# Optimization experiments

Measured on AMD Instinct MI355X. Metric: run time of the kernel, lower is better.

## Reference

```python
import jax, jax.numpy as jnp
import numpy as np
import math

B, S, H = 1, 2048, 4096
NH, HD = 32, 128  # heads, head_dim
ROPE_THETA = 10000.0
SINK = 4
RECENT_RATIO = 0.1


def setup_inputs() -> dict:
    key = jax.random.key(0)
    ks = jax.random.split(key, 5)
    scale = 0.02
    return {
        "hidden_states": jax.random.normal(ks[0], (B, S, H), jnp.float32),
        "Wq": jax.random.normal(ks[1], (H, H), jnp.float32) * scale,
        "Wk": jax.random.normal(ks[2], (H, H), jnp.float32) * scale,
        "Wv": jax.random.normal(ks[3], (H, H), jnp.float32) * scale,
        "Wo": jax.random.normal(ks[4], (H, H), jnp.float32) * scale,
        "position_ids": jnp.arange(S, dtype=jnp.int64)[None, :],
    }


def _rope(x, cos, sin):
    # x: [B, NH, S, HD]; rotate_half = cat(-x2, x1)
    half = x.shape[-1] // 2
    rot = jnp.concatenate([-x[..., half:], x[..., :half]], axis=-1)
    return x * cos + rot * sin


def reference(hidden_states, Wq, Wk, Wv, Wo, position_ids):
    b, s, h = hidden_states.shape
    # projections (torch Linear: x @ W^T), split heads -> [B, NH, S, HD]
    q = (hidden_states @ Wq.T).reshape(b, s, NH, HD).transpose(0, 2, 1, 3)
    k = (hidden_states @ Wk.T).reshape(b, s, NH, HD).transpose(0, 2, 1, 3)
    v = (hidden_states @ Wv.T).reshape(b, s, NH, HD).transpose(0, 2, 1, 3)

    # rotary embeddings from position_ids
    inv_freq = 1.0 / (ROPE_THETA ** (jnp.arange(0, HD, 2, dtype=jnp.float32) / HD))
    freqs = position_ids.astype(jnp.float32)[..., None] * inv_freq  # [B, S, HD/2]
    emb = jnp.concatenate([freqs, freqs], axis=-1)                   # [B, S, HD]
    cos = jnp.cos(emb)[:, None, :, :]
    sin = jnp.sin(emb)[:, None, :, :]
    q = _rope(q, cos, sin)
    k = _rope(k, cos, sin)

    # causal attention
    scores = jnp.einsum('bhqd,bhkd->bhqk', q, k) / math.sqrt(HD)
    neg = jnp.finfo(scores.dtype).min
    causal = jnp.tril(jnp.ones((s, s), dtype=bool))
    scores = jnp.where(causal[None, None], scores, neg)
    attn = jax.nn.softmax(scores, axis=-1)
    out = jnp.einsum('bhqk,bhkd->bhqd', attn, v)
    out = out.transpose(0, 2, 1, 3).reshape(b, s, h)
    attn_output = out @ Wo.T

    # H2O streaming cache eviction: sink (first 4) + recent window KV
    recent = int(s * RECENT_RATIO)
    k_evicted = jnp.concatenate([k[:, :, :SINK, :], k[:, :, s - recent:, :]], axis=2)
    v_evicted = jnp.concatenate([v[:, :, :SINK, :], v[:, :, s - recent:, :]], axis=2)
    return attn_output, k_evicted, v_evicted
```

## Files before the change

kernel.cpp:

```cpp
#include <hip/hip_runtime.h>
#include <hip/hip_bf16.h>

typedef __bf16 bf16;
typedef __bf16 bf16x4 __attribute__((ext_vector_type(4)));
typedef __bf16 bf16x8 __attribute__((ext_vector_type(8)));
typedef float f32x4 __attribute__((ext_vector_type(4)));

#define MFMA16(a, b, c) __builtin_amdgcn_mfma_f32_16x16x32_bf16(a, b, c, 0, 0, 0)

constexpr int S_LEN = 2048;
constexpr int HDIM = 4096;
constexpr int NHEADS = 32;
constexpr int HEADD = 128;
constexpr int SINKN = 4;
constexpr int RECENT = 204;
constexpr int EVROWS = SINKN + RECENT;
constexpr float QSCALE = 0.08838834764831845f;

constexpr int JOBS_PER_HEAD = 40;
constexpr int SLOTS_PER_HEAD = 36;
constexpr size_t SLOT_BYTES = 33792;

__device__ inline bf16x8 cvt8(const float* p) {
    float4 a = *(const float4*)p;
    float4 b = *(const float4*)(p + 4);
    return bf16x8{(bf16)a.x, (bf16)a.y, (bf16)a.z, (bf16)a.w,
                  (bf16)b.x, (bf16)b.y, (bf16)b.z, (bf16)b.w};
}

__device__ inline void gload16(const bf16* g, bf16* l) {
    __builtin_amdgcn_global_load_lds(
        (const __attribute__((address_space(1))) unsigned int*)g,
        (__attribute__((address_space(3))) unsigned int*)l, 16, 0, 0);
}

__global__ __launch_bounds__(256) void cvt_kernel(const float* __restrict__ in,
                                                  bf16* __restrict__ out, int n8) {
    int i = blockIdx.x * 256 + threadIdx.x;
    if (i >= n8) return;
    *(bf16x8*)(out + (size_t)i * 8) = cvt8(in + (size_t)i * 8);
}

__device__ __forceinline__ void stage_b256(const bf16* __restrict__ Bp, bf16* dst,
                                           int K, int kc, int tid) {
#pragma unroll
    for (int r = 0; r < 2; ++r) {
        int idx = r * 512 + tid;
        int row = idx >> 3;
        int gs = (idx & 7) ^ (row & 7);
        gload16(Bp + (size_t)row * K + kc + gs * 8, dst + idx * 8);
    }
}
template <int MH>
__device__ __forceinline__ void stage_a256(const bf16* __restrict__ Ap, bf16* dst,
                                           int K, int kc, int tid) {
#pragma unroll
    for (int r = 0; r < 2; ++r) {
        int idx = r * 512 + tid;
        int row = idx >> 3;
        int gs = (idx & 7) ^ (row & 7);
        gload16(Ap + (size_t)(MH * 128 + row) * K + kc + gs * 8,
                dst + MH * 8192 + idx * 8);
    }
}
template <int MH>
__device__ __forceinline__ void lda256(const bf16* buf, int wm, int lg, int lr,
                                       bf16x8 (&af)[2][2]) {
#pragma unroll
    for (int mt = 0; mt < 2; ++mt)
#pragma unroll
        for (int kk = 0; kk < 2; ++kk)
            af[mt][kk] = *(const bf16x8*)&buf[MH * 8192 + (wm * 32 + mt * 16 + lr) * 64 +
                                              (((kk * 4 + lg) ^ (lr & 7)) * 8)];
}
__device__ __forceinline__ void ldb256(const bf16* buf, int wn, int lg, int lr,
                                       bf16x8 (&bfr)[4][2]) {
#pragma unroll
    for (int nt = 0; nt < 4; ++nt)
#pragma unroll
        for (int kk = 0; kk < 2; ++kk)
            bfr[nt][kk] = *(const bf16x8*)&buf[(wn * 64 + nt * 16 + lr) * 64 +
                                               (((kk * 4 + lg) ^ (lr & 7)) * 8)];
}
template <int MH>
__device__ __forceinline__ void mma256(const bf16x8 (&af)[2][2], const bf16x8 (&bfr)[4][2],
                                       f32x4 (&acc)[2][2][4]) {
#pragma unroll
    for (int mt = 0; mt < 2; ++mt)
#pragma unroll
        for (int nt = 0; nt < 4; ++nt)
#pragma unroll
            for (int kk = 0; kk < 2; ++kk)
                acc[MH][mt][nt] = MFMA16(af[mt][kk], bfr[nt][kk], acc[MH][mt][nt]);
}

template <bool C_IS_F32>
__global__ __launch_bounds__(512, 2) void gemm256(const bf16* __restrict__ A,
                                                  const bf16* __restrict__ B,
                                                  void* __restrict__ Cv,
                                                  int M, int N, int K) {
    __shared__ bf16 Abuf[2][256 * 64];
    __shared__ bf16 Bbuf[2][128 * 64];

    const int tid = threadIdx.x;
    const int lane = tid & 63, wid = tid >> 6;
    const int wm = wid >> 1, wn = wid & 1;
    const int lg = lane >> 4, lr = lane & 15;

    const int bid = blockIdx.x;
    const int bx = (bid & 7) * 4 + (bid >> 6);
    const int by = (bid >> 3) & 7;
    const int m0 = by * 256, n0 = bx * 128;

    const bf16* Ap = A + (size_t)m0 * K;
    const bf16* Bp = B + (size_t)n0 * K;

    f32x4 acc[2][2][4] = {};
    bf16x8 af[2][2], bfr[4][2];

    stage_b256(Bp, Bbuf[0], K, 0, tid);
    stage_a256<0>(Ap, Abuf[0], K, 0, tid);
    stage_a256<1>(Ap, Abuf[0], K, 0, tid);
    asm volatile("s_waitcnt vmcnt(2)" ::: "memory");
    __builtin_amdgcn_s_barrier();

    const bf16 *Ard = Abuf[0], *Brd = Bbuf[0];
    bf16 *Awr = Abuf[1], *Bwr = Bbuf[1];

    const int NT = K / 64;
    for (int t = 0; t < NT - 1; ++t) {
        const int kc = (t + 1) * 64;
        ldb256(Brd, wn, lg, lr, bfr);
        lda256<0>(Ard, wm, lg, lr, af);
        stage_b256(Bp, Bwr, K, kc, tid);
        stage_a256<0>(Ap, Awr, K, kc, tid);
        __builtin_amdgcn_s_barrier();
        asm volatile("s_waitcnt lgkmcnt(0)" ::: "memory");
        __builtin_amdgcn_sched_barrier(0);
        __builtin_amdgcn_s_setprio(1);
        mma256<0>(af, bfr, acc);
        __builtin_amdgcn_s_setprio(0);
        asm volatile("s_waitcnt vmcnt(4)" ::: "memory");
        __builtin_amdgcn_s_barrier();
        lda256<1>(Ard, wm, lg, lr, af);
        stage_a256<1>(Ap, Awr, K, kc, tid);
        __builtin_amdgcn_s_barrier();
        asm volatile("s_waitcnt lgkmcnt(0)" ::: "memory");
        __builtin_amdgcn_sched_barrier(0);
        __builtin_amdgcn_s_setprio(1);
        mma256<1>(af, bfr, acc);
        __builtin_amdgcn_s_setprio(0);
        asm volatile("s_waitcnt vmcnt(2)" ::: "memory");
        __builtin_amdgcn_s_barrier();
        const bf16* tA = Ard; Ard = Awr; Awr = (bf16*)tA;
        const bf16* tB = Brd; Brd = Bwr; Bwr = (bf16*)tB;
    }
    asm volatile("s_waitcnt vmcnt(0)" ::: "memory");
    __builtin_amdgcn_s_barrier();
    ldb256(Brd, wn, lg, lr, bfr);
    lda256<0>(Ard, wm, lg, lr, af);
    mma256<0>(af, bfr, acc);
    lda256<1>(Ard, wm, lg, lr, af);
    mma256<1>(af, bfr, acc);

#pragma unroll
    for (int mh = 0; mh < 2; ++mh)
#pragma unroll
        for (int mt = 0; mt < 2; ++mt)
#pragma unroll
            for (int nt = 0; nt < 4; ++nt)
#pragma unroll
                for (int r = 0; r < 4; ++r) {
                    int row = m0 + mh * 128 + wm * 32 + mt * 16 + lg * 4 + r;
                    int col = n0 + wn * 64 + nt * 16 + lr;
                    if constexpr (C_IS_F32)
                        ((float*)Cv)[(size_t)row * N + col] = acc[mh][mt][nt][r];
                    else
                        ((bf16*)Cv)[(size_t)row * N + col] = (bf16)acc[mh][mt][nt][r];
                }
}

__global__ __launch_bounds__(256) void rope_kernel(bf16* __restrict__ q,
                                                   bf16* __restrict__ k) {
    const int s = blockIdx.x;
    const int t = threadIdx.x;
    const int hh = t >> 3;
    const int i0 = (t & 7) << 3;
    const size_t base = (size_t)s * HDIM + hh * HEADD;

    bf16x8 q1 = *(bf16x8*)(q + base + i0);
    bf16x8 q2 = *(bf16x8*)(q + base + 64 + i0);
    bf16x8 k1 = *(bf16x8*)(k + base + i0);
    bf16x8 k2 = *(bf16x8*)(k + base + 64 + i0);
    bf16x8 q1o, q2o, k1o, k2o;
    const float pos = (float)s;
#pragma unroll
    for (int j = 0; j < 8; ++j) {
        float f = pos * exp2f((float)(i0 + j) * (-0.2076205059304602f));
        float sn, cs;
        sincosf(f, &sn, &cs);
        float x1 = (float)q1[j], x2 = (float)q2[j];
        q1o[j] = (bf16)((x1 * cs - x2 * sn) * QSCALE);
        q2o[j] = (bf16)((x2 * cs + x1 * sn) * QSCALE);
        x1 = (float)k1[j]; x2 = (float)k2[j];
        k1o[j] = (bf16)(x1 * cs - x2 * sn);
        k2o[j] = (bf16)(x2 * cs + x1 * sn);
    }
    *(bf16x8*)(q + base + i0) = q1o;
    *(bf16x8*)(q + base + 64 + i0) = q2o;
    *(bf16x8*)(k + base + i0) = k1o;
    *(bf16x8*)(k + base + 64 + i0) = k2o;
}

__global__ __launch_bounds__(256) void transpose_v(const bf16* __restrict__ v,
                                                   bf16* __restrict__ vt) {
    __shared__ bf16 tile[64][136];
    const int h = blockIdx.x;
    const int s0 = blockIdx.y * 64;
    const int tid = threadIdx.x;
#pragma unroll
    for (int j = 0; j < 4; ++j) {
        int ch = tid + 256 * j;
        int row = ch >> 4, c8 = (ch & 15) << 3;
        *(bf16x8*)&tile[row][c8] =
            *(const bf16x8*)(v + (size_t)(s0 + row) * HDIM + h * HEADD + c8);
    }
    __syncthreads();
#pragma unroll
    for (int j = 0; j < 4; ++j) {
        int ch = tid + 256 * j;
        int d = ch >> 3, s8 = (ch & 7) << 3;
        bf16x8 w;
#pragma unroll
        for (int i = 0; i < 8; ++i) w[i] = tile[s8 + i][d];
        *(bf16x8*)(vt + ((size_t)h * HEADD + d) * S_LEN + s0 + s8) = w;
    }
}

__global__ __launch_bounds__(256, 2) void attn_kernel(const bf16* __restrict__ q,
                                                      const bf16* __restrict__ k,
                                                      const bf16* __restrict__ vt,
                                                      bf16* __restrict__ o,
                                                      char* __restrict__ partials) {
    __shared__ bf16 K_lds[2][64 * 128];
    __shared__ bf16 V_lds[128 * 64];
    __shared__ bf16 P_lds[4][32 * 72];

    const int tid = threadIdx.x;
    const int lane = tid & 63, wid = tid >> 6;
    const int lg = lane >> 4, lr = lane & 15;

    const int bj = blockIdx.x;
    const int h = bj / JOBS_PER_HEAD;
    const int within = JOBS_PER_HEAD - 1 - (bj % JOBS_PER_HEAD);
    int qb, chunk, nj;
    if (within < 4)       { qb = within; chunk = 0; nj = 1; }
    else if (within < 12) { int u2 = within - 4;  qb = 4  + (u2 >> 1); chunk = u2 & 1;        nj = 2; }
    else if (within < 24) { int u2 = within - 12; int q3 = u2 / 3; qb = 8 + q3; chunk = u2 - 3 * q3; nj = 3; }
    else                  { int u2 = within - 24; qb = 12 + (u2 >> 2); chunk = u2 & 3;        nj = 4; }
    const int q0 = qb * 128;
    const int ntiles = 2 * qb + 2;
    const int tb = chunk * 8;
    const int te = min(tb + 8, ntiles);

    bf16x8 aq[2][4];
#pragma unroll
    for (int rs = 0; rs < 2; ++rs)
#pragma unroll
        for (int dc = 0; dc < 4; ++dc)
            aq[rs][dc] = *(const bf16x8*)(q + (size_t)(q0 + wid * 32 + rs * 16 + lr) * HDIM +
                                          h * HEADD + dc * 32 + lg * 8);

    f32x4 oacc[2][8] = {};
    float m_[2] = {-1e30f, -1e30f};
    float l_[2] = {0.f, 0.f};
    bf16* pw = &P_lds[wid][0];

    {
        const int kv0 = tb << 6;
#pragma unroll
        for (int i = 0; i < 4; ++i) {
            const int c = wid * 4 + i;
            const int krow = 4 * c + (lane >> 4);
            const int kg = (lane & 15) ^ (krow & 7);
            gload16(k + (size_t)(kv0 + krow) * HDIM + h * HEADD + kg * 8,
                    &K_lds[0][c * 512]);
        }
    }

    int cur = 0;
    for (int t = tb; t < te; ++t) {
        const int kv0 = t << 6;
#pragma unroll
        for (int i = 0; i < 4; ++i) {
            const int c = wid * 4 + i;
            const int vrow = 8 * c + (lane >> 3);
            const int vg = (lane & 7) ^ (vrow & 7);
            gload16(vt + (size_t)(h * HEADD + vrow) * S_LEN + kv0 + vg * 8,
                    &V_lds[c * 512]);
        }
        if (t + 1 < te) {
            const int kvn = (t + 1) << 6;
#pragma unroll
            for (int i = 0; i < 4; ++i) {
                const int c = wid * 4 + i;
                const int krow = 4 * c + (lane >> 4);
                const int kg = (lane & 15) ^ (krow & 7);
                gload16(k + (size_t)(kvn + krow) * HDIM + h * HEADD + kg * 8,
                        &K_lds[cur ^ 1][c * 512]);
            }
            asm volatile("s_waitcnt vmcnt(8)" ::: "memory");
        } else {
            asm volatile("s_waitcnt vmcnt(4)" ::: "memory");
        }
        __builtin_amdgcn_s_barrier();
        __builtin_amdgcn_sched_barrier(0);

        const bf16* Kb = &K_lds[cur][0];
        f32x4 st[2][4] = {};
#pragma unroll
        for (int kt = 0; kt < 4; ++kt) {
            bf16x8 kf[4];
#pragma unroll
            for (int dc = 0; dc < 4; ++dc)
                kf[dc] = *(const bf16x8*)&Kb[(kt * 16 + lr) * 128 +
                                             (((dc * 4 + lg) ^ (lr & 7)) * 8)];
#pragma unroll
            for (int dc = 0; dc < 4; ++dc) {
                st[0][kt] = MFMA16(kf[dc], aq[0][dc], st[0][kt]);
                st[1][kt] = MFMA16(kf[dc], aq[1][dc], st[1][kt]);
            }
        }

#pragma unroll
        for (int rs = 0; rs < 2; ++rs) {
            const int qr0 = q0 + wid * 32 + rs * 16;
            float v[16];
            if ((kv0 + 63) > qr0) {
                const int qidx = qr0 + lr;
#pragma unroll
                for (int kt = 0; kt < 4; ++kt)
#pragma unroll
                    for (int r = 0; r < 4; ++r) {
                        float x = st[rs][kt][r];
                        if (kv0 + kt * 16 + lg * 4 + r > qidx) x = -1e30f;
                        v[kt * 4 + r] = x;
                    }
            } else {
#pragma unroll
                for (int kt = 0; kt < 4; ++kt)
#pragma unroll
                    for (int r = 0; r < 4; ++r) v[kt * 4 + r] = st[rs][kt][r];
            }
            float pm = v[0];
#pragma unroll
            for (int i = 1; i < 16; ++i) pm = fmaxf(pm, v[i]);
            pm = fmaxf(pm, __shfl_xor(pm, 16));
            pm = fmaxf(pm, __shfl_xor(pm, 32));

            if (__any(pm > m_[rs] + 8.0f)) {
                float mn = fmaxf(m_[rs], pm);
                float sc = __expf(m_[rs] - mn);
                m_[rs] = mn;
                l_[rs] *= sc;
                float scb[4];
#pragma unroll
                for (int r = 0; r < 4; ++r)
                    scb[r] = __uint_as_float(__builtin_amdgcn_ds_bpermute(
                        (lg * 4 + r) * 4, __float_as_uint(sc)));
#pragma unroll
                for (int dt = 0; dt < 8; ++dt)
#pragma unroll
                    for (int r = 0; r < 4; ++r) oacc[rs][dt][r] *= scb[r];
            }
            const float mn = m_[rs];
            float rsum = 0.f;
#pragma unroll
            for (int kt = 0; kt < 4; ++kt) {
                bf16x4 pk;
#pragma unroll
                for (int r = 0; r < 4; ++r) {
                    float p = __expf(v[kt * 4 + r] - mn);
                    rsum += p;
                    pk[r] = (bf16)p;
                }
                *(bf16x4*)&pw[(rs * 16 + lr) * 72 + kt * 16 + lg * 4] = pk;
            }
            rsum += __shfl_xor(rsum, 16);
            rsum += __shfl_xor(rsum, 32);
            l_[rs] += rsum;
        }

        if (t + 1 < te) asm volatile("s_waitcnt vmcnt(4)" ::: "memory");
        else            asm volatile("s_waitcnt vmcnt(0)" ::: "memory");
        __builtin_amdgcn_s_barrier();
        __builtin_amdgcn_sched_barrier(0);

        bf16x8 pa[2][2];
#pragma unroll
        for (int rs = 0; rs < 2; ++rs)
#pragma unroll
            for (int kt2 = 0; kt2 < 2; ++kt2)
                pa[rs][kt2] = *(const bf16x8*)&pw[(rs * 16 + lr) * 72 + kt2 * 32 + lg * 8];
#pragma unroll
        for (int kt2 = 0; kt2 < 2; ++kt2)
#pragma unroll
            for (int dt = 0; dt < 8; ++dt) {
                bf16x8 bv = *(const bf16x8*)&V_lds[(dt * 16 + lr) * 64 +
                                                   (((kt2 * 4 + lg) ^ (lr & 7)) * 8)];
                oacc[0][dt] = MFMA16(pa[0][kt2], bv, oacc[0][dt]);
                oacc[1][dt] = MFMA16(pa[1][kt2], bv, oacc[1][dt]);
            }

        __builtin_amdgcn_s_barrier();
        __builtin_amdgcn_sched_barrier(0);
        cur ^= 1;
    }

    if (nj == 1) {
#pragma unroll
        for (int rs = 0; rs < 2; ++rs) {
            float lb[4];
#pragma unroll
            for (int r = 0; r < 4; ++r)
                lb[r] = __uint_as_float(__builtin_amdgcn_ds_bpermute(
                    (lg * 4 + r) * 4, __float_as_uint(l_[rs])));
#pragma unroll
            for (int r = 0; r < 4; ++r) {
                float inv = 1.0f / lb[r];
                const int row = q0 + wid * 32 + rs * 16 + lg * 4 + r;
#pragma unroll
                for (int dt = 0; dt < 8; ++dt)
                    o[(size_t)row * HDIM + h * HEADD + dt * 16 + lr] =
                        (bf16)(oacc[rs][dt][r] * inv);
            }
        }
    } else {
        const int sb = (qb < 8) ? (qb - 4) * 2 : (qb < 12) ? 8 + (qb - 8) * 3
                                                           : 20 + (qb - 12) * 4;
        char* slotp = partials + ((size_t)h * SLOTS_PER_HEAD + sb + chunk) * SLOT_BYTES;
        bf16* Op = (bf16*)slotp;
        float* mp = (float*)(slotp + 32768);
        float* lp = mp + 128;
#pragma unroll
        for (int rs = 0; rs < 2; ++rs) {
            const int rowl = wid * 32 + rs * 16;
#pragma unroll
            for (int r = 0; r < 4; ++r)
#pragma unroll
                for (int dt = 0; dt < 8; ++dt)
                    Op[(rowl + lg * 4 + r) * HEADD + dt * 16 + lr] = (bf16)oacc[rs][dt][r];
            if (lg == 0) { mp[rowl + lr] = m_[rs]; lp[rowl + lr] = l_[rs]; }
        }
    }
}

__global__ __launch_bounds__(256) void combine_kernel(const char* __restrict__ partials,
                                                      bf16* __restrict__ o) {
    const int h = blockIdx.x;
    const int qb = 4 + blockIdx.y;
    const int nj = (2 * qb + 9) / 8;
    const int sb = (qb < 8) ? (qb - 4) * 2 : (qb < 12) ? 8 + (qb - 8) * 3
                                                       : 20 + (qb - 12) * 4;
    const char* base = partials + ((size_t)h * SLOTS_PER_HEAD + sb) * SLOT_BYTES;

    const int row = threadIdx.x >> 1;
    const int d0 = (threadIdx.x & 1) * 64;

    float mc[4], lc[4];
    float M = -1e30f;
    for (int c = 0; c < nj; ++c) {
        const char* sp = base + (size_t)c * SLOT_BYTES;
        mc[c] = ((const float*)(sp + 32768))[row];
        lc[c] = ((const float*)(sp + 33280))[row];
        M = fmaxf(M, mc[c]);
    }
    float denom = 0.f;
    float acc[64] = {};
    for (int c = 0; c < nj; ++c) {
        float wgt = __expf(mc[c] - M);
        denom += wgt * lc[c];
        const bf16* Op = (const bf16*)(base + (size_t)c * SLOT_BYTES);
#pragma unroll
        for (int j = 0; j < 8; ++j) {
            bf16x8 a = *(const bf16x8*)&Op[row * HEADD + d0 + j * 8];
#pragma unroll
            for (int e = 0; e < 8; ++e) acc[j * 8 + e] += wgt * (float)a[e];
        }
    }
    float inv = 1.0f / denom;
    bf16* dst = o + (size_t)(qb * 128 + row) * HDIM + h * HEADD + d0;
#pragma unroll
    for (int j = 0; j < 8; ++j) {
        bf16x8 w;
#pragma unroll
        for (int e = 0; e < 8; ++e) w[e] = (bf16)(acc[j * 8 + e] * inv);
        *(bf16x8*)&dst[j * 8] = w;
    }
}

__global__ __launch_bounds__(256) void evict_kernel(const bf16* __restrict__ k,
                                                    const bf16* __restrict__ v,
                                                    float* __restrict__ out) {
    const int total = NHEADS * EVROWS * HEADD;
    int idx = blockIdx.x * 256 + threadIdx.x;
    if (idx >= 2 * total) return;
    const int which = idx / total;
    const int rem = idx % total;
    const int hh = rem / (EVROWS * HEADD);
    const int i = (rem / HEADD) % EVROWS;
    const int d = rem % HEADD;
    const int s = (i < SINKN) ? i : (S_LEN - RECENT) + (i - SINKN);
    const bf16* src = which ? v : k;
    out[(size_t)S_LEN * HDIM + (size_t)which * total + rem] =
        (float)src[(size_t)s * HDIM + hh * HEADD + d];
}

extern "C" void kernel_launch(void* const* d_in, const int* in_sizes, int n_in,
                              void* d_out, int out_size, void* d_ws, size_t ws_size,
                              hipStream_t stream) {
    const float* hs = (const float*)d_in[0];
    const float* Wq = (const float*)d_in[1];
    const float* Wk = (const float*)d_in[2];
    const float* Wv = (const float*)d_in[3];
    const float* Wo = (const float*)d_in[4];
    float* out = (float*)d_out;

    const size_t MB = 1024 * 1024;
    char* w = (char*)d_ws;
    bf16* hs_bf = (bf16*)(w);
    bf16* W_bf  = (bf16*)(w + 16 * MB);
    char* part  = w;
    bf16* q_ws  = (bf16*)(w + 48 * MB);
    bf16* k_ws  = (bf16*)(w + 64 * MB);
    bf16* v_ws  = (bf16*)(w + 80 * MB);
    bf16* vt_ws = (bf16*)(w + 96 * MB);
    bf16* o_ws  = q_ws;

    const int nW8 = HDIM * HDIM / 8;
    const int nH8 = S_LEN * HDIM / 8;

    cvt_kernel<<<(nH8 + 255) / 256, 256, 0, stream>>>(hs, hs_bf, nH8);

    cvt_kernel<<<(nW8 + 255) / 256, 256, 0, stream>>>(Wq, W_bf, nW8);
    gemm256<false><<<256, 512, 0, stream>>>(hs_bf, W_bf, q_ws, S_LEN, HDIM, HDIM);
    cvt_kernel<<<(nW8 + 255) / 256, 256, 0, stream>>>(Wk, W_bf, nW8);
    gemm256<false><<<256, 512, 0, stream>>>(hs_bf, W_bf, k_ws, S_LEN, HDIM, HDIM);
    cvt_kernel<<<(nW8 + 255) / 256, 256, 0, stream>>>(Wv, W_bf, nW8);
    gemm256<false><<<256, 512, 0, stream>>>(hs_bf, W_bf, v_ws, S_LEN, HDIM, HDIM);

    rope_kernel<<<S_LEN, 256, 0, stream>>>(q_ws, k_ws);
    transpose_v<<<dim3(NHEADS, S_LEN / 64), 256, 0, stream>>>(v_ws, vt_ws);

    evict_kernel<<<(2 * NHEADS * EVROWS * HEADD + 255) / 256, 256, 0, stream>>>(k_ws, v_ws, out);

    attn_kernel<<<NHEADS * JOBS_PER_HEAD, 256, 0, stream>>>(q_ws, k_ws, vt_ws, o_ws, part);
    combine_kernel<<<dim3(NHEADS, 12), 256, 0, stream>>>(part, o_ws);

    cvt_kernel<<<(nW8 + 255) / 256, 256, 0, stream>>>(Wo, W_bf, nW8);
    gemm256<true><<<256, 512, 0, stream>>>(o_ws, W_bf, out, S_LEN, HDIM, HDIM);
}
```

Baseline: 439.2 us.

## Triple-buffer LDS in GEMM with two-tile-deep global prefetch

The GEMM main loop moves from double-buffered LDS staging, with the A half-tiles split into two phases, to a triple-buffered scheme. Global loads run two k-tiles ahead of compute, and each iteration now needs one wait and two barriers instead of four barriers. All A and B fragments for a tile are loaded at once into separate register sets, so both MFMA halves issue back to back. The cost is about 50% more LDS per block and extra fragment registers, which may cause spills under the 512-thread launch bound and makes the hand-written vmcnt counts fragile.

```diff
diff --git a/kernel.cpp b/kernel.cpp
--- a/kernel.cpp
+++ b/kernel.cpp
@@ -99,8 +99,8 @@
                                                   const bf16* __restrict__ B,
                                                   void* __restrict__ Cv,
                                                   int M, int N, int K) {
-    __shared__ bf16 Abuf[2][256 * 64];
-    __shared__ bf16 Bbuf[2][128 * 64];
+    __shared__ bf16 Abuf[3][256 * 64];
+    __shared__ bf16 Bbuf[3][128 * 64];
 
     const int tid = threadIdx.x;
     const int lane = tid & 63, wid = tid >> 6;
@@ -116,52 +116,44 @@
     const bf16* Bp = B + (size_t)n0 * K;
 
     f32x4 acc[2][2][4] = {};
-    bf16x8 af[2][2], bfr[4][2];
+    bf16x8 af0[2][2], af1[2][2], bfr[4][2];
 
     stage_b256(Bp, Bbuf[0], K, 0, tid);
     stage_a256<0>(Ap, Abuf[0], K, 0, tid);
     stage_a256<1>(Ap, Abuf[0], K, 0, tid);
-    asm volatile("s_waitcnt vmcnt(2)" ::: "memory");
-    __builtin_amdgcn_s_barrier();
-
-    const bf16 *Ard = Abuf[0], *Brd = Bbuf[0];
-    bf16 *Awr = Abuf[1], *Bwr = Bbuf[1];
+    stage_b256(Bp, Bbuf[1], K, 64, tid);
+    stage_a256<0>(Ap, Abuf[1], K, 64, tid);
+    stage_a256<1>(Ap, Abuf[1], K, 64, tid);
 
     const int NT = K / 64;
-    for (int t = 0; t < NT - 1; ++t) {
-        const int kc = (t + 1) * 64;
-        ldb256(Brd, wn, lg, lr, bfr);
-        lda256<0>(Ard, wm, lg, lr, af);
-        stage_b256(Bp, Bwr, K, kc, tid);
-        stage_a256<0>(Ap, Awr, K, kc, tid);
+    for (int t = 0; t < NT; ++t) {
+        const int cur = t % 3;
+        if (t + 2 < NT) {
+            const int nb = (t + 2) % 3;
+            const int kc = (t + 2) * 64;
+            stage_b256(Bp, Bbuf[nb], K, kc, tid);
+            stage_a256<0>(Ap, Abuf[nb], K, kc, tid);
+            stage_a256<1>(Ap, Abuf[nb], K, kc, tid);
+            asm volatile("s_waitcnt vmcnt(12)" ::: "memory");
+        } else if (t + 1 < NT) {
+            asm volatile("s_waitcnt vmcnt(6)" ::: "memory");
+        } else {
+            asm volatile("s_waitcnt vmcnt(0)" ::: "memory");
+        }
         __builtin_amdgcn_s_barrier();
+        __builtin_amdgcn_sched_barrier(0);
+
+        lda256<0>(Abuf[cur], wm, lg, lr, af0);
+        lda256<1>(Abuf[cur], wm, lg, lr, af1);
+        ldb256(Bbuf[cur], wn, lg, lr, bfr);
         asm volatile("s_waitcnt lgkmcnt(0)" ::: "memory");
         __builtin_amdgcn_sched_barrier(0);
         __builtin_amdgcn_s_setprio(1);
-        mma256<0>(af, bfr, acc);
+        mma256<0>(af0, bfr, acc);
+        mma256<1>(af1, bfr, acc);
         __builtin_amdgcn_s_setprio(0);
-        asm volatile("s_waitcnt vmcnt(4)" ::: "memory");
         __builtin_amdgcn_s_barrier();
-        lda256<1>(Ard, wm, lg, lr, af);
-        stage_a256<1>(Ap, Awr, K, kc, tid);
-        __builtin_amdgcn_s_barrier();
-        asm volatile("s_waitcnt lgkmcnt(0)" ::: "memory");
-        __builtin_amdgcn_sched_barrier(0);
-        __builtin_amdgcn_s_setprio(1);
-        mma256<1>(af, bfr, acc);
-        __builtin_amdgcn_s_setprio(0);
-        asm volatile("s_waitcnt vmcnt(2)" ::: "memory");
-        __builtin_amdgcn_s_barrier();
-        const bf16* tA = Ard; Ard = Awr; Awr = (bf16*)tA;
-        const bf16* tB = Brd; Brd = Bwr; Bwr = (bf16*)tB;
-    }
-    asm volatile("s_waitcnt vmcnt(0)" ::: "memory");
-    __builtin_amdgcn_s_barrier();
-    ldb256(Brd, wn, lg, lr, bfr);
-    lda256<0>(Ard, wm, lg, lr, af);
-    mma256<0>(af, bfr, acc);
-    lda256<1>(Ard, wm, lg, lr, af);
-    mma256<1>(af, bfr, acc);
+    }
 
 #pragma unroll
     for (int mh = 0; mh < 2; ++mh)
```

After: 531.3 us. +21.0%, slower.

## Fuse next weight fp32->bf16 conversion into GEMM via extra converter warps

Applied to the files above, without the earlier changes.

Adds two extra wavefronts per GEMM block that convert the next projection's fp32 weights to bf16 into a double-buffered workspace while the MFMA warps compute the current GEMM. The converter warps issue matching barriers to stay in lockstep. This removes three standalone conversion kernels and their serialization between GEMMs. In exchange it needs more workspace (a fallback path is kept), raises block size to 640 threads (possible occupancy and register pressure), and depends on exact barrier counts matching the main loop.

```diff
diff --git a/kernel.cpp b/kernel.cpp
--- a/kernel.cpp
+++ b/kernel.cpp
@@ -94,15 +94,39 @@
                 acc[MH][mt][nt] = MFMA16(af[mt][kk], bfr[nt][kk], acc[MH][mt][nt]);
 }
 
-template <bool C_IS_F32>
-__global__ __launch_bounds__(512, 2) void gemm256(const bf16* __restrict__ A,
-                                                  const bf16* __restrict__ B,
-                                                  void* __restrict__ Cv,
-                                                  int M, int N, int K) {
+template <bool C_IS_F32, bool FUSE>
+__global__ __launch_bounds__(FUSE ? 640 : 512, 2) void gemm256(
+        const bf16* __restrict__ A, const bf16* __restrict__ B,
+        void* __restrict__ Cv, int M, int N, int K,
+        const float* __restrict__ Wsrc, bf16* __restrict__ Wdst) {
     __shared__ bf16 Abuf[2][256 * 64];
     __shared__ bf16 Bbuf[2][128 * 64];
 
     const int tid = threadIdx.x;
+    const int NT = K / 64;
+
+    if constexpr (FUSE) {
+        if (tid >= 512) {
+            const int ct = tid - 512;
+            const size_t base = (size_t)blockIdx.x * 8192 + ct;
+            {
+                size_t i = base;
+                *(bf16x8*)(Wdst + i * 8) = cvt8(Wsrc + i * 8);
+            }
+            __builtin_amdgcn_s_barrier();
+            for (int t = 0; t < NT - 1; ++t) {
+                size_t i = base + (size_t)(t + 1) * 128;
+                *(bf16x8*)(Wdst + i * 8) = cvt8(Wsrc + i * 8);
+                __builtin_amdgcn_s_barrier();
+                __builtin_amdgcn_s_barrier();
+                __builtin_amdgcn_s_barrier();
+                __builtin_amdgcn_s_barrier();
+            }
+            __builtin_amdgcn_s_barrier();
+            return;
+        }
+    }
+
     const int lane = tid & 63, wid = tid >> 6;
     const int wm = wid >> 1, wn = wid & 1;
     const int lg = lane >> 4, lr = lane & 15;
@@ -127,7 +151,6 @@
     const bf16 *Ard = Abuf[0], *Brd = Bbuf[0];
     bf16 *Awr = Abuf[1], *Bwr = Bbuf[1];
 
-    const int NT = K / 64;
     for (int t = 0; t < NT - 1; ++t) {
         const int kc = (t + 1) * 64;
         ldb256(Brd, wn, lg, lr, bfr);
@@ -528,35 +551,60 @@
 
     const size_t MB = 1024 * 1024;
     char* w = (char*)d_ws;
-    bf16* hs_bf = (bf16*)(w);
-    bf16* W_bf  = (bf16*)(w + 16 * MB);
-    char* part  = w;
-    bf16* q_ws  = (bf16*)(w + 48 * MB);
-    bf16* k_ws  = (bf16*)(w + 64 * MB);
-    bf16* v_ws  = (bf16*)(w + 80 * MB);
-    bf16* vt_ws = (bf16*)(w + 96 * MB);
-    bf16* o_ws  = q_ws;
-
     const int nW8 = HDIM * HDIM / 8;
     const int nH8 = S_LEN * HDIM / 8;
 
-    cvt_kernel<<<(nH8 + 255) / 256, 256, 0, stream>>>(hs, hs_bf, nH8);
-
-    cvt_kernel<<<(nW8 + 255) / 256, 256, 0, stream>>>(Wq, W_bf, nW8);
-    gemm256<false><<<256, 512, 0, stream>>>(hs_bf, W_bf, q_ws, S_LEN, HDIM, HDIM);
-    cvt_kernel<<<(nW8 + 255) / 256, 256, 0, stream>>>(Wk, W_bf, nW8);
-    gemm256<false><<<256, 512, 0, stream>>>(hs_bf, W_bf, k_ws, S_LEN, HDIM, HDIM);
-    cvt_kernel<<<(nW8 + 255) / 256, 256, 0, stream>>>(Wv, W_bf, nW8);
-    gemm256<false><<<256, 512, 0, stream>>>(hs_bf, W_bf, v_ws, S_LEN, HDIM, HDIM);
-
-    rope_kernel<<<S_LEN, 256, 0, stream>>>(q_ws, k_ws);
-    transpose_v<<<dim3(NHEADS, S_LEN / 64), 256, 0, stream>>>(v_ws, vt_ws);
-
-    evict_kernel<<<(2 * NHEADS * EVROWS * HEADD + 255) / 256, 256, 0, stream>>>(k_ws, v_ws, out);
-
-    attn_kernel<<<NHEADS * JOBS_PER_HEAD, 256, 0, stream>>>(q_ws, k_ws, vt_ws, o_ws, part);
-    combine_kernel<<<dim3(NHEADS, 12), 256, 0, stream>>>(part, o_ws);
-
-    cvt_kernel<<<(nW8 + 255) / 256, 256, 0, stream>>>(Wo, W_bf, nW8);
-    gemm256<true><<<256, 512, 0, stream>>>(o_ws, W_bf, out, S_LEN, HDIM, HDIM);
-}
+    if (ws_size >= 187 * MB) {
+        char* part  = w;
+        bf16* hs_bf = (bf16*)(w + 39 * MB);
+        bf16* buf0  = (bf16*)(w + 55 * MB);
+        bf16* buf1  = (bf16*)(w + 89 * MB);
+        bf16* q_ws  = (bf16*)(w + 123 * MB);
+        bf16* k_ws  = (bf16*)(w + 139 * MB);
+        bf16* v_ws  = (bf16*)(w + 155 * MB);
+        bf16* vt_ws = (bf16*)(w + 171 * MB);
+        bf16* o_ws  = q_ws;
+
+        cvt_kernel<<<(nH8 + 255) / 256, 256, 0, stream>>>(hs, hs_bf, nH8);
+        cvt_kernel<<<(nW8 + 255) / 256, 256, 0, stream>>>(Wq, buf0, nW8);
+
+        gemm256<false, true><<<256, 640, 0, stream>>>(hs_bf, buf0, q_ws, S_LEN, HDIM, HDIM, Wk, buf1);
+        gemm256<false, true><<<256, 640, 0, stream>>>(hs_bf, buf1, k_ws, S_LEN, HDIM, HDIM, Wv, buf0);
+        gemm256<false, true><<<256, 640, 0, stream>>>(hs_bf, buf0, v_ws, S_LEN, HDIM, HDIM, Wo, buf1);
+
+        rope_kernel<<<S_LEN, 256, 0, stream>>>(q_ws, k_ws);
+        transpose_v<<<dim3(NHEADS, S_LEN / 64), 256, 0, stream>>>(v_ws, vt_ws);
+        evict_kernel<<<(2 * NHEADS * EVROWS * HEADD + 255) / 256, 256, 0, stream>>>(k_ws, v_ws, out);
+        attn_kernel<<<NHEADS * JOBS_PER_HEAD, 256, 0, stream>>>(q_ws, k_ws, vt_ws, o_ws, part);
+        combine_kernel<<<dim3(NHEADS, 12), 256, 0, stream>>>(part, o_ws);
+
+        gemm256<true, false><<<256, 512, 0, stream>>>(o_ws, buf1, out, S_LEN, HDIM, HDIM, nullptr, nullptr);
+    } else {
+        bf16* hs_bf = (bf16*)(w);
+        bf16* W_bf  = (bf16*)(w + 16 * MB);
+        char* part  = w;
+        bf16* q_ws  = (bf16*)(w + 48 * MB);
+        bf16* k_ws  = (bf16*)(w + 64 * MB);
+        bf16* v_ws  = (bf16*)(w + 80 * MB);
+        bf16* vt_ws = (bf16*)(w + 96 * MB);
+        bf16* o_ws  = q_ws;
+
+        cvt_kernel<<<(nH8 + 255) / 256, 256, 0, stream>>>(hs, hs_bf, nH8);
+
+        cvt_kernel<<<(nW8 + 255) / 256, 256, 0, stream>>>(Wq, W_bf, nW8);
+        gemm256<false, false><<<256, 512, 0, stream>>>(hs_bf, W_bf, q_ws, S_LEN, HDIM, HDIM, nullptr, nullptr);
+        cvt_kernel<<<(nW8 + 255) / 256, 256, 0, stream>>>(Wk, W_bf, nW8);
+        gemm256<false, false><<<256, 512, 0, stream>>>(hs_bf, W_bf, k_ws, S_LEN, HDIM, HDIM, nullptr, nullptr);
+        cvt_kernel<<<(nW8 + 255) / 256, 256, 0, stream>>>(Wv, W_bf, nW8);
+        gemm256<false, false><<<256, 512, 0, stream>>>(hs_bf, W_bf, v_ws, S_LEN, HDIM, HDIM, nullptr, nullptr);
+
+        rope_kernel<<<S_LEN, 256, 0, stream>>>(q_ws, k_ws);
+        transpose_v<<<dim3(NHEADS, S_LEN / 64), 256, 0, stream>>>(v_ws, vt_ws);
+        evict_kernel<<<(2 * NHEADS * EVROWS * HEADD + 255) / 256, 256, 0, stream>>>(k_ws, v_ws, out);
+        attn_kernel<<<NHEADS * JOBS_PER_HEAD, 256, 0, stream>>>(q_ws, k_ws, vt_ws, o_ws, part);
+        combine_kernel<<<dim3(NHEADS, 12), 256, 0, stream>>>(part, o_ws);
+
+        cvt_kernel<<<(nW8 + 255) / 256, 256, 0, stream>>>(Wo, W_bf, nW8);
+        gemm256<true, false><<<256, 512, 0, stream>>>(o_ws, W_bf, out, S_LEN, HDIM, HDIM, nullptr, nullptr);
+    }
+}
```

After: 444.2 us. Within noise of the previous version (+1.1%).
